# Kernel optimization log

Hardware: AMD Instinct MI355X
Metric: run time of the kernel (lower is better)

Reference implementation:

```python
import jax, jax.numpy as jnp
import numpy as np

B, T, D, K = 16, 8192, 64, 1024


def setup_inputs() -> dict:
    key = jax.random.key(0)
    k1, k2 = jax.random.split(key)
    x = jax.random.normal(k1, (B, T, D, 1), dtype=jnp.float32)
    weight = jax.random.normal(k2, (K, D), dtype=jnp.float32)
    return {"x": x, "weight": weight}


def reference(x, weight):
    # x: [B, T, D, 1] -> squeeze trailing dim -> [B, T, D]
    xs = jnp.squeeze(x, axis=-1)
    x2 = jnp.sum(xs * xs, axis=-1, keepdims=True)          # [B, T, 1]
    e2 = jnp.sum(weight * weight, axis=-1)                 # [K]
    xe = jnp.einsum('btd,kd->btk', xs, weight)             # [B, T, K]
    dist2 = x2 - 2.0 * xe + e2                             # [B, T, K]
    indices = jnp.argmin(dist2, axis=-1)                   # [B, T] int
    quantized = jnp.take(weight, indices, axis=0)          # [B, T, D]
    return quantized, indices
```

## Files before the change

### kernel.cpp

```cpp
#include <hip/hip_runtime.h>

#define MTOK  131072
#define DIMD  64
#define KCODE 1024
#define TPB   128

typedef __bf16 bf16x8 __attribute__((ext_vector_type(8)));
typedef float  f32x4  __attribute__((ext_vector_type(4)));

__device__ __forceinline__ f32x4 mfma16(bf16x8 a, bf16x8 b, f32x4 c) {
    return __builtin_amdgcn_mfma_f32_16x16x32_bf16(a, b, c, 0, 0, 0);
}

__device__ __forceinline__ void g2l16(const void* g, void* l) {
    __builtin_amdgcn_global_load_lds(
        (const __attribute__((address_space(1))) unsigned int*)g,
        (__attribute__((address_space(3))) unsigned int*)l, 16, 0, 0);
}

__global__ __launch_bounds__(256) void prep_kernel(
    const float* __restrict__ w, __bf16* __restrict__ wpk,
    float* __restrict__ e2n, float* __restrict__ e2) {
    int b   = blockIdx.x;
    int tid = threadIdx.x;
    if (b < 64) {
        int cb  = b;
        int win = tid >> 6, lane = tid & 63;
        int q = lane >> 4, m = lane & 15;
        int k = cb * 16 + m;
        int d0 = (win & 1) * 32 + q * 8;
        const float* src = w + (size_t)k * DIMD + d0;
        float4 v0 = *(const float4*)(src);
        float4 v1 = *(const float4*)(src + 4);
        float f[8] = {v0.x, v0.y, v0.z, v0.w, v1.x, v1.y, v1.z, v1.w};
        bf16x8 o;
#pragma unroll
        for (int j = 0; j < 8; ++j) {
            __bf16 h = (__bf16)f[j];
            o[j] = (win < 2) ? h : (__bf16)(f[j] - (float)h);
        }
        *(bf16x8*)(wpk + ((size_t)(cb * 4 + win) * 64 + lane) * 8) = o;
    } else {
        int k2 = (b - 64) * 256 + tid;
        const float4* row = (const float4*)(w + (size_t)k2 * DIMD);
        float s = 0.f;
#pragma unroll
        for (int i = 0; i < 16; ++i) {
            float4 v = row[i];
            s = fmaf(v.x, v.x, s); s = fmaf(v.y, v.y, s);
            s = fmaf(v.z, v.z, s); s = fmaf(v.w, v.w, s);
        }
        e2[k2]  = s;
        e2n[k2] = -0.5f * s;
    }
}

__global__ __launch_bounds__(256, 4) void vq_main(
    const float* __restrict__ x, const float* __restrict__ wfull,
    const __bf16* __restrict__ wpk, const float* __restrict__ e2n_g,
    const float* __restrict__ e2_g, float* __restrict__ out) {

    __shared__ __align__(16) __bf16 ldsW[2][8192];
    __shared__ __align__(16) float  ldsE[KCODE];

    const int tid  = threadIdx.x;
    const int blk  = blockIdx.x;
    const int lane = tid & 63;
    const int wv   = tid >> 6;
    const int q    = lane >> 4;
    const int m    = lane & 15;
    const size_t tok0 = (size_t)blk * TPB + wv * 32;

    {
        const char* gw = (const char*)wpk + (size_t)wv * 4096 + (size_t)lane * 16;
        char* lw = (char*)&ldsW[0][0] + wv * 4096 + lane * 16;
#pragma unroll
        for (int j = 0; j < 4; ++j)
            g2l16(gw + j * 1024, lw + j * 1024);
        g2l16((const char*)e2n_g + (size_t)wv * 1024 + lane * 16,
              (char*)ldsE + wv * 1024 + lane * 16);
    }

    bf16x8 bx[2][4];
#pragma unroll
    for (int tg = 0; tg < 2; ++tg) {
        const float* xr = x + (tok0 + tg * 16 + m) * DIMD;
#pragma unroll
        for (int h = 0; h < 2; ++h) {
            float4 v0 = *(const float4*)(xr + h * 32 + q * 8);
            float4 v1 = *(const float4*)(xr + h * 32 + q * 8 + 4);
            float f[8] = {v0.x, v0.y, v0.z, v0.w, v1.x, v1.y, v1.z, v1.w};
            bf16x8 hi, lo;
#pragma unroll
            for (int j = 0; j < 8; ++j) {
                __bf16 hh = (__bf16)f[j];
                hi[j] = hh;
                lo[j] = (__bf16)(f[j] - (float)hh);
            }
            bx[tg][h]     = hi;
            bx[tg][2 + h] = lo;
        }
    }

    float b1[2], b2[2]; int i1[2];
#pragma unroll
    for (int tg = 0; tg < 2; ++tg) { b1[tg] = -3e38f; b2[tg] = -3e38f; i1[tg] = 0; }

    auto step = [&](bf16x8 f0, bf16x8 f1, bf16x8 f2, bf16x8 f3, f32x4 ee, int cbase) {
#pragma unroll
        for (int tg = 0; tg < 2; ++tg) {
            f32x4 t = mfma16(f0, bx[tg][0], ee);
            t = mfma16(f1, bx[tg][1], t);
            t = mfma16(f0, bx[tg][2], t);
            t = mfma16(f1, bx[tg][3], t);
            t = mfma16(f2, bx[tg][0], t);
            t = mfma16(f3, bx[tg][1], t);
#pragma unroll
            for (int r = 0; r < 4; ++r) {
                float a   = t[r];
                int idxv  = cbase + q * 4 + r;
                bool gt   = a > b1[tg];
                i1[tg] = gt ? idxv : i1[tg];
                b2[tg] = __builtin_amdgcn_fmed3f(a, b1[tg], b2[tg]);
                b1[tg] = fmaxf(a, b1[tg]);
            }
        }
    };

    __syncthreads();

    for (int c = 0; c < 16; ++c) {
        if (c + 1 < 16) {
            const char* gw = (const char*)wpk + (size_t)(c + 1) * 16384
                           + (size_t)wv * 4096 + (size_t)lane * 16;
            char* lw = (char*)&ldsW[(c + 1) & 1][0] + wv * 4096 + lane * 16;
#pragma unroll
            for (int j = 0; j < 4; ++j)
                g2l16(gw + j * 1024, lw + j * 1024);
        }
        const __bf16* wb = &ldsW[c & 1][0] + lane * 8;
#pragma unroll
        for (int cbl = 0; cbl < 4; ++cbl) {
            bf16x8 a0 = *(const bf16x8*)(wb + cbl * 2048 + 0);
            bf16x8 a1 = *(const bf16x8*)(wb + cbl * 2048 + 512);
            bf16x8 a2 = *(const bf16x8*)(wb + cbl * 2048 + 1024);
            bf16x8 a3 = *(const bf16x8*)(wb + cbl * 2048 + 1536);
            f32x4  ee = *(const f32x4*)&ldsE[c * 64 + cbl * 16 + q * 4];
            step(a0, a1, a2, a3, ee, (c * 4 + cbl) * 16);
        }
        __syncthreads();
    }

    float B1f[2], B2f[2]; int I1f[2];
#pragma unroll
    for (int tg = 0; tg < 2; ++tg) {
        float B1 = b1[tg], B2 = b2[tg]; int I1 = i1[tg];
#pragma unroll
        for (int mask = 16; mask <= 32; mask <<= 1) {
            float ob1 = __shfl_xor(B1, mask);
            float ob2 = __shfl_xor(B2, mask);
            int   oi  = __shfl_xor(I1, mask);
            bool take = (ob1 > B1) || (ob1 == B1 && oi < I1);
            B2 = fmaxf(fminf(ob1, B1), fmaxf(ob2, B2));
            I1 = take ? oi : I1;
            B1 = fmaxf(ob1, B1);
        }
        B1f[tg] = B1; B2f[tg] = B2; I1f[tg] = I1;
    }

    int myidx;
    {
        int src = lane & 15;
        int v0 = __shfl(I1f[0], src);
        int v1 = __shfl(I1f[1], src);
        myidx = ((lane >> 4) & 1) ? v1 : v0;
    }

#pragma unroll
    for (int tg = 0; tg < 2; ++tg) {
        unsigned long long msk =
            __ballot((lane < 16) && (B1f[tg] - B2f[tg] < 2e-3f));
        while (msk) {
            int mm = __ffsll((unsigned long long)msk) - 1;
            msk &= msk - 1;
            int tloc = tg * 16 + mm;
            const float4* xr = (const float4*)(x + (tok0 + tloc) * DIMD);
            float bv = 3e38f; int bi = 0;
            for (int j = 0; j < 16; ++j) {
                int k = lane * 16 + j;
                const float4* wr = (const float4*)(wfull + (size_t)k * DIMD);
                float s = 0.f;
#pragma unroll
                for (int i = 0; i < 16; ++i) {
                    float4 xv = xr[i], wv4 = wr[i];
                    s = fmaf(xv.x, wv4.x, s); s = fmaf(xv.y, wv4.y, s);
                    s = fmaf(xv.z, wv4.z, s); s = fmaf(xv.w, wv4.w, s);
                }
                float dv = fmaf(-2.f, s, e2_g[k]);
                if (dv < bv) { bv = dv; bi = k; }
            }
#pragma unroll
            for (int mask2 = 1; mask2 <= 32; mask2 <<= 1) {
                float ov = __shfl_xor(bv, mask2);
                int   oi = __shfl_xor(bi, mask2);
                bool take = (ov < bv) || (ov == bv && oi < bi);
                bv = take ? ov : bv;
                bi = take ? oi : bi;
            }
            myidx = (lane == tloc) ? bi : myidx;
        }
    }

    if (lane < 32)
        out[(size_t)MTOK * DIMD + tok0 + lane] = (float)myidx;

    {
        float* obase = out + tok0 * DIMD;
#pragma unroll
        for (int j = 0; j < 8; ++j) {
            int srcl = j * 4 + (lane >> 4);
            int gi   = __shfl(myidx, srcl);
            float4 v = *(const float4*)(wfull + (size_t)gi * DIMD + (lane & 15) * 4);
            *(float4*)(obase + j * 256 + lane * 4) = v;
        }
    }
}

extern "C" void kernel_launch(void* const* d_in, const int* in_sizes, int n_in,
                              void* d_out, int out_size, void* d_ws, size_t ws_size,
                              hipStream_t stream) {
    const float* x = (const float*)d_in[0];
    const float* w = (const float*)d_in[1];
    float* out = (float*)d_out;

    __bf16* wpk = (__bf16*)d_ws;
    float*  e2n = (float*)((char*)d_ws + 262144);
    float*  e2  = (float*)((char*)d_ws + 266240);

    prep_kernel<<<68, 256, 0, stream>>>(w, wpk, e2n, e2);
    vq_main<<<MTOK / TPB, 256, 0, stream>>>(x, w, wpk, e2n, e2, out);
}
```

Baseline: 145.2 us.

## Software-pipeline LDS codebook loads and interleave MFMA chains with priority hints

Restructures the inner codebook loop so that LDS fragments for the next sub-block are double-buffered in registers and loaded while the current MFMAs run. The two token-group MFMA chains are interleaved to hide accumulation latency, and s_setprio is raised around the MFMA burst. The final-iteration barrier is skipped, and output stores become nontemporal. These changes target LDS latency stalls and MFMA dependency stalls, at the cost of more register pressure, which could hurt occupancy under the 4-wave launch bound.

```diff
diff --git a/kernel.cpp b/kernel.cpp
--- a/kernel.cpp
+++ b/kernel.cpp
@@ -106,30 +106,21 @@
 #pragma unroll
     for (int tg = 0; tg < 2; ++tg) { b1[tg] = -3e38f; b2[tg] = -3e38f; i1[tg] = 0; }
 
-    auto step = [&](bf16x8 f0, bf16x8 f1, bf16x8 f2, bf16x8 f3, f32x4 ee, int cbase) {
-#pragma unroll
-        for (int tg = 0; tg < 2; ++tg) {
-            f32x4 t = mfma16(f0, bx[tg][0], ee);
-            t = mfma16(f1, bx[tg][1], t);
-            t = mfma16(f0, bx[tg][2], t);
-            t = mfma16(f1, bx[tg][3], t);
-            t = mfma16(f2, bx[tg][0], t);
-            t = mfma16(f3, bx[tg][1], t);
-#pragma unroll
-            for (int r = 0; r < 4; ++r) {
-                float a   = t[r];
-                int idxv  = cbase + q * 4 + r;
-                bool gt   = a > b1[tg];
-                i1[tg] = gt ? idxv : i1[tg];
-                b2[tg] = __builtin_amdgcn_fmed3f(a, b1[tg], b2[tg]);
-                b1[tg] = fmaxf(a, b1[tg]);
-            }
-        }
-    };
-
     __syncthreads();
 
     for (int c = 0; c < 16; ++c) {
+        const __bf16* wb = &ldsW[c & 1][0] + lane * 8;
+        const int eb = c * 64 + q * 4;
+
+        bf16x8 A0[2], A1[2], A2[2], A3[2];
+        f32x4  EE[2];
+
+        A0[0] = *(const bf16x8*)(wb + 0);
+        A1[0] = *(const bf16x8*)(wb + 512);
+        A2[0] = *(const bf16x8*)(wb + 1024);
+        A3[0] = *(const bf16x8*)(wb + 1536);
+        EE[0] = *(const f32x4*)&ldsE[eb];
+
         if (c + 1 < 16) {
             const char* gw = (const char*)wpk + (size_t)(c + 1) * 16384
                            + (size_t)wv * 4096 + (size_t)lane * 16;
@@ -138,17 +129,62 @@
             for (int j = 0; j < 4; ++j)
                 g2l16(gw + j * 1024, lw + j * 1024);
         }
-        const __bf16* wb = &ldsW[c & 1][0] + lane * 8;
+
+        A0[1] = *(const bf16x8*)(wb + 2048);
+        A1[1] = *(const bf16x8*)(wb + 2048 + 512);
+        A2[1] = *(const bf16x8*)(wb + 2048 + 1024);
+        A3[1] = *(const bf16x8*)(wb + 2048 + 1536);
+        EE[1] = *(const f32x4*)&ldsE[eb + 16];
+
 #pragma unroll
         for (int cbl = 0; cbl < 4; ++cbl) {
-            bf16x8 a0 = *(const bf16x8*)(wb + cbl * 2048 + 0);
-            bf16x8 a1 = *(const bf16x8*)(wb + cbl * 2048 + 512);
-            bf16x8 a2 = *(const bf16x8*)(wb + cbl * 2048 + 1024);
-            bf16x8 a3 = *(const bf16x8*)(wb + cbl * 2048 + 1536);
-            f32x4  ee = *(const f32x4*)&ldsE[c * 64 + cbl * 16 + q * 4];
-            step(a0, a1, a2, a3, ee, (c * 4 + cbl) * 16);
-        }
-        __syncthreads();
+            const int cur = cbl & 1;
+            f32x4 t0, t1;
+            __builtin_amdgcn_s_setprio(1);
+            t0 = mfma16(A0[cur], bx[0][0], EE[cur]);
+            t1 = mfma16(A0[cur], bx[1][0], EE[cur]);
+            t0 = mfma16(A1[cur], bx[0][1], t0);
+            t1 = mfma16(A1[cur], bx[1][1], t1);
+            t0 = mfma16(A0[cur], bx[0][2], t0);
+            t1 = mfma16(A0[cur], bx[1][2], t1);
+            t0 = mfma16(A1[cur], bx[0][3], t0);
+            t1 = mfma16(A1[cur], bx[1][3], t1);
+            t0 = mfma16(A2[cur], bx[0][0], t0);
+            t1 = mfma16(A2[cur], bx[1][0], t1);
+            t0 = mfma16(A3[cur], bx[0][1], t0);
+            t1 = mfma16(A3[cur], bx[1][1], t1);
+            __builtin_amdgcn_s_setprio(0);
+
+            if (cbl < 2) {
+                const int nx = cbl + 2;
+                A0[cur] = *(const bf16x8*)(wb + nx * 2048);
+                A1[cur] = *(const bf16x8*)(wb + nx * 2048 + 512);
+                A2[cur] = *(const bf16x8*)(wb + nx * 2048 + 1024);
+                A3[cur] = *(const bf16x8*)(wb + nx * 2048 + 1536);
+                EE[cur] = *(const f32x4*)&ldsE[eb + nx * 16];
+            }
+
+            const int cbase = (c * 4 + cbl) * 16;
+#pragma unroll
+            for (int r = 0; r < 4; ++r) {
+                float a  = t0[r];
+                int iv   = cbase + q * 4 + r;
+                bool gt  = a > b1[0];
+                i1[0] = gt ? iv : i1[0];
+                b2[0] = __builtin_amdgcn_fmed3f(a, b1[0], b2[0]);
+                b1[0] = fmaxf(a, b1[0]);
+            }
+#pragma unroll
+            for (int r = 0; r < 4; ++r) {
+                float a  = t1[r];
+                int iv   = cbase + q * 4 + r;
+                bool gt  = a > b1[1];
+                i1[1] = gt ? iv : i1[1];
+                b2[1] = __builtin_amdgcn_fmed3f(a, b1[1], b2[1]);
+                b1[1] = fmaxf(a, b1[1]);
+            }
+        }
+        if (c + 1 < 16) __syncthreads();
     }
 
     float B1f[2], B2f[2]; int I1f[2];
@@ -212,7 +248,8 @@
     }
 
     if (lane < 32)
-        out[(size_t)MTOK * DIMD + tok0 + lane] = (float)myidx;
+        __builtin_nontemporal_store((float)myidx,
+                                    out + (size_t)MTOK * DIMD + tok0 + lane);
 
     {
         float* obase = out + tok0 * DIMD;
@@ -220,8 +257,8 @@
         for (int j = 0; j < 8; ++j) {
             int srcl = j * 4 + (lane >> 4);
             int gi   = __shfl(myidx, srcl);
-            float4 v = *(const float4*)(wfull + (size_t)gi * DIMD + (lane & 15) * 4);
-            *(float4*)(obase + j * 256 + lane * 4) = v;
+            f32x4 v = *(const f32x4*)(wfull + (size_t)gi * DIMD + (lane & 15) * 4);
+            __builtin_nontemporal_store(v, (f32x4*)(obase + j * 256 + lane * 4));
         }
     }
 }
```

After: 142.5 us. Within noise of the previous version (-1.9%).
